# Optimization experiments

Hardware: AMD Instinct MI355X
Metric: run time of the kernel (lower is better)

Reference implementation:

```python
import jax, jax.numpy as jnp
import numpy as np

B_, L_, D_ = 2, 1024, 2048
E_, N_, R_, K_ = 4096, 16, 128, 4
EPS = 1e-5


def setup_inputs() -> dict:
    key = jax.random.key(0)
    ks = jax.random.split(key, 12)
    s = lambda i, shape, scale=0.02: jax.random.normal(ks[i], shape, jnp.float32) * scale
    # dt bias init as in the module: inv_dt = dt + log(-expm1(-dt)), dt ~ logU[1e-3, 0.1]
    dt = jnp.exp(jax.random.uniform(ks[10], (E_,)) * (np.log(0.1) - np.log(0.001)) + np.log(0.001))
    inv_dt = dt + jnp.log(-jnp.expm1(-dt))
    return {
        'resid': jax.random.normal(ks[0], (B_, L_, D_), jnp.float32),
        'norm_w': jnp.ones((D_,), jnp.float32),
        'skip_w': s(1, (E_, D_)),
        'in_w': s(2, (E_, D_)),
        'conv_w': s(3, (E_, K_), 0.2),
        'conv_b': jnp.zeros((E_,), jnp.float32),
        'wd1': s(4, (R_, E_)),
        'wd2': s(5, (E_, R_), R_ ** -0.5),
        'wd2_b': inv_dt,
        'wB': s(6, (N_, E_)),
        'wC': s(7, (N_, E_)),
        'A_log': jnp.log(jnp.broadcast_to(jnp.arange(1, N_ + 1, dtype=jnp.float32), (E_, N_))),
        'W_D': jnp.ones((E_,), jnp.float32),
        'out_w': s(8, (D_, E_)),
    }


def _forward(resid, norm_w, skip_w, in_w, conv_w, conv_b, wd1, wd2, wd2_b,
             wB, wC, A_log, W_D, out_w):
    B, L, D = resid.shape
    E, K = conv_w.shape
    N = A_log.shape[1]
    # RMSNorm
    rn = resid * jax.lax.rsqrt(jnp.mean(resid * resid, -1, keepdims=True) + EPS) * norm_w
    skip = rn @ skip_w.T                       # [B,L,E] gate branch (z)
    x_in = rn @ in_w.T                         # [B,L,E]
    # depthwise causal conv1d (pad left K-1, truncate to L), then SiLU
    xp = jnp.pad(x_in, ((0, 0), (K - 1, 0), (0, 0)))
    conv = conv_b + sum(xp[:, k:k + L, :] * conv_w[:, k] for k in range(K))
    x = jax.nn.silu(conv)                      # [B,L,E] ssm input
    # low-rank delta, input-dependent B/C
    delta = jax.nn.softplus((x @ wd1.T) @ wd2.T + wd2_b)   # [B,L,E]
    A = -jnp.exp(A_log)                        # [E,N]
    Bm = x @ wB.T                              # [B,L,N]
    Cm = x @ wC.T                              # [B,L,N]

    def step(h, inp):
        d_l, b_l, c_l, x_l = inp               # [B,E],[B,N],[B,N],[B,E]
        h = jnp.exp(d_l[:, :, None] * A) * h + (d_l * x_l)[:, :, None] * b_l[:, None, :]
        y_l = jnp.einsum('ben,bn->be', h, c_l)
        return h, y_l

    h0 = jnp.zeros((B, E, N), resid.dtype)
    xs = (delta.transpose(1, 0, 2), Bm.transpose(1, 0, 2),
          Cm.transpose(1, 0, 2), x.transpose(1, 0, 2))
    _, ys = jax.lax.scan(step, h0, xs)         # ys: [L,B,E]
    y = ys.transpose(1, 0, 2) + x * W_D        # skip connection via D
    y = y * jax.nn.silu(skip)                  # gating
    return resid + y @ out_w.T                 # out_proj + residual


def reference(resid, norm_w, skip_w, in_w, conv_w, conv_b, wd1, wd2, wd2_b,
              wB, wC, A_log, W_D, out_w):
    return _forward(resid, norm_w, skip_w, in_w, conv_w, conv_b, wd1, wd2,
                    wd2_b, wB, wC, A_log, W_D, out_w)
```

## Files before the change

kernel.cpp:

```cpp
#include <hip/hip_runtime.h>
#include <stdint.h>

#define NB 2
#define NL 1024
#define ND 2048
#define NE 4096
#define NN 16
#define NR 128
#define NKC 4
#define NBL (NB*NL)
#define EPSV 1e-5f
#define SEG_T 256
#define SCAN_T 32

typedef __attribute__((ext_vector_type(4))) float f32x4;
typedef __attribute__((ext_vector_type(8))) short short8;
typedef __attribute__((ext_vector_type(8))) unsigned short ushort8;
typedef __attribute__((ext_vector_type(4))) unsigned short ushort4_t;
typedef __attribute__((ext_vector_type(2))) unsigned short ushort2_t;

__device__ __forceinline__ unsigned short f2bf(float f) {
  union { float f; unsigned u; } v; v.f = f;
  unsigned r = v.u + 0x7FFFu + ((v.u >> 16) & 1u);
  return (unsigned short)(r >> 16);
}

__device__ __forceinline__ float bf2f(unsigned short u) {
  union { unsigned u; float f; } v; v.u = (unsigned)u << 16; return v.f;
}

__device__ __forceinline__ void load_lds16(const void* g, void* l) {
  __builtin_amdgcn_global_load_lds((const __attribute__((address_space(1))) void*)g,
                                   (__attribute__((address_space(3))) void*)l,
                                   16, 0, 0);
}

template<int CTRL>
__device__ __forceinline__ float dpp_mov(float v) {
  return __int_as_float(__builtin_amdgcn_update_dpp(
      0, __float_as_int(v), CTRL, 0xF, 0xF, true));
}

__global__ void rmsnorm_kernel(const float* __restrict__ resid,
                               const float* __restrict__ nw,
                               unsigned short* __restrict__ rn) {
  int row = blockIdx.x;
  int tid = threadIdx.x;
  const float* r = resid + (size_t)row * ND;
  f32x4 v0 = *(const f32x4*)(r + tid * 8);
  f32x4 v1 = *(const f32x4*)(r + tid * 8 + 4);
  float vals[8];
#pragma unroll
  for (int i = 0; i < 4; ++i) { vals[i] = v0[i]; vals[4 + i] = v1[i]; }
  float ss = 0.f;
#pragma unroll
  for (int i = 0; i < 8; ++i) ss += vals[i] * vals[i];
  for (int o = 32; o > 0; o >>= 1) ss += __shfl_down(ss, o);
  __shared__ float ps[4];
  if ((tid & 63) == 0) ps[tid >> 6] = ss;
  __syncthreads();
  float tot = ps[0] + ps[1] + ps[2] + ps[3];
  float scale = rsqrtf(tot / (float)ND + EPSV);
  ushort8 o8;
#pragma unroll
  for (int i = 0; i < 8; ++i) o8[i] = f2bf(vals[i] * scale * nw[tid * 8 + i]);
  *(ushort8*)(rn + (size_t)row * ND + tid * 8) = o8;
}

__global__ void cast_bf16_kernel(const float* __restrict__ in,
                                 unsigned short* __restrict__ out, int n8) {
  int i = blockIdx.x * blockDim.x + threadIdx.x;
  if (i >= n8) return;
  f32x4 a = *(const f32x4*)(in + (size_t)i * 8);
  f32x4 b = *(const f32x4*)(in + (size_t)i * 8 + 4);
  ushort8 o;
#pragma unroll
  for (int j = 0; j < 4; ++j) { o[j] = f2bf(a[j]); o[4 + j] = f2bf(b[j]); }
  *(ushort8*)(out + (size_t)i * 8) = o;
}

__global__ void build_wcat_kernel(const float* __restrict__ wd1,
                                  const float* __restrict__ wB,
                                  const float* __restrict__ wC,
                                  unsigned short* __restrict__ out) {
  int i = blockIdx.x * blockDim.x + threadIdx.x;
  if (i >= 256 * NE / 8) return;
  int col8 = i & (NE / 8 - 1);
  int row = i >> 9;
  const float* src = nullptr; int srow = 0;
  if (row < 128)      { src = wd1; srow = row; }
  else if (row < 144) { src = wB;  srow = row - 128; }
  else if (row < 160) { src = wC;  srow = row - 144; }
  ushort8 o;
  if (src) {
    f32x4 a = *(const f32x4*)(src + (size_t)srow * NE + col8 * 8);
    f32x4 b = *(const f32x4*)(src + (size_t)srow * NE + col8 * 8 + 4);
#pragma unroll
    for (int j = 0; j < 4; ++j) { o[j] = f2bf(a[j]); o[4 + j] = f2bf(b[j]); }
  } else {
#pragma unroll
    for (int j = 0; j < 8; ++j) o[j] = 0;
  }
  *(ushort8*)(out + (size_t)row * NE + col8 * 8) = o;
}

__global__ __launch_bounds__(512, 2)
void gemm256_fused(const unsigned short* __restrict__ A,
                   const unsigned short* __restrict__ B,
                   float* __restrict__ Gout,
                   unsigned short* __restrict__ Xout) {
  const int K = 2048, NH = K / 32;
  __shared__ unsigned short Asl[4][8192];
  __shared__ unsigned short Bsl[4][8192];
  int tid = threadIdx.x;
  int w = tid >> 6, lane = tid & 63;
  int wm = w >> 2, wn = w & 3;
  int lr = lane & 15, kg8 = (lane >> 4) * 8;
  int m0 = blockIdx.y * 256, n0 = blockIdx.x * 256;

  const unsigned short* ga = A + (size_t)(m0 + (tid >> 2)) * K + (tid & 3) * 8;
  const unsigned short* gb = B + (size_t)(n0 + (tid >> 2)) * K + (tid & 3) * 8;
  char* ldsA0 = (char*)&Asl[0][0] + w * 1024;
  char* ldsB0 = (char*)&Bsl[0][0] + w * 1024;

  auto stageA = [&](int h) {
    int slot = h & 3, k0 = h * 32;
    load_lds16(ga + k0, ldsA0 + slot * 16384);
    load_lds16(ga + k0 + (size_t)128 * K, ldsA0 + slot * 16384 + 8192);
  };
  auto stageB = [&](int h) {
    int slot = h & 3, k0 = h * 32;
    load_lds16(gb + k0, ldsB0 + slot * 16384);
    load_lds16(gb + k0 + (size_t)128 * K, ldsB0 + slot * 16384 + 8192);
  };

  f32x4 acc[8][4];
#pragma unroll
  for (int i = 0; i < 8; ++i)
#pragma unroll
    for (int j = 0; j < 4; ++j) acc[i][j] = (f32x4){0.f, 0.f, 0.f, 0.f};

  stageA(0); stageB(0); stageA(1); stageB(1); stageA(2); stageB(2);
  asm volatile("s_waitcnt vmcnt(8)" ::: "memory");
  __builtin_amdgcn_s_barrier();

  for (int h = 0; h < NH; ++h) {
    int slot = h & 3;
    const unsigned short* As_ = &Asl[slot][0];
    const unsigned short* Bs_ = &Bsl[slot][0];
    int arow = wm * 128 + lr;
    int brow = wn * 64 + lr;
    short8 a[8], b[4];
#pragma unroll
    for (int i = 0; i < 4; ++i)
      a[i] = *(const short8*)&As_[(arow + i * 16) * 32 + kg8];
#pragma unroll
    for (int j = 0; j < 4; ++j)
      b[j] = *(const short8*)&Bs_[(brow + j * 16) * 32 + kg8];
    if (h + 3 < NH) stageA(h + 3);
    __builtin_amdgcn_s_barrier();
    __builtin_amdgcn_s_setprio(1);
#pragma unroll
    for (int i = 0; i < 4; ++i)
#pragma unroll
      for (int j = 0; j < 4; ++j)
        acc[i][j] = __builtin_amdgcn_mfma_f32_16x16x32_bf16(a[i], b[j], acc[i][j], 0, 0, 0);
    __builtin_amdgcn_s_setprio(0);
    __builtin_amdgcn_s_barrier();
#pragma unroll
    for (int i = 0; i < 4; ++i)
      a[4 + i] = *(const short8*)&As_[(arow + (4 + i) * 16) * 32 + kg8];
    if (h + 3 < NH) stageB(h + 3);
    __builtin_amdgcn_s_barrier();
    __builtin_amdgcn_s_setprio(1);
#pragma unroll
    for (int i = 0; i < 4; ++i)
#pragma unroll
      for (int j = 0; j < 4; ++j)
        acc[4 + i][j] = __builtin_amdgcn_mfma_f32_16x16x32_bf16(a[4 + i], b[j], acc[4 + i][j], 0, 0, 0);
    __builtin_amdgcn_s_setprio(0);
    if (h < NH - 3)       { asm volatile("s_waitcnt vmcnt(8)" ::: "memory"); }
    else if (h == NH - 3) { asm volatile("s_waitcnt vmcnt(4)" ::: "memory"); }
    else if (h == NH - 2) { asm volatile("s_waitcnt vmcnt(0)" ::: "memory"); }
    __builtin_amdgcn_s_barrier();
  }

  int rbase = m0 + wm * 128 + (lane >> 4) * 4;
  int cbase = n0 + wn * 64 + (lane & 15);
  bool isg = (n0 < 4096);
#pragma unroll
  for (int mf = 0; mf < 8; ++mf) {
#pragma unroll
    for (int nf = 0; nf < 4; ++nf) {
      int col = cbase + nf * 16;
#pragma unroll
      for (int rr = 0; rr < 4; ++rr) {
        int row = rbase + mf * 16 + rr;
        float v = acc[mf][nf][rr];
        if (isg) Gout[(size_t)row * 4096 + col] = v / (1.f + __expf(-v));
        else     Xout[(size_t)row * 4096 + (col - 4096)] = f2bf(v);
      }
    }
  }
}

template<int MODE>
__global__ __launch_bounds__(256)
void gemm_bt(const unsigned short* __restrict__ A,
             const unsigned short* __restrict__ B,
             float* __restrict__ C,
             int M, int N, int K, int ksteps_per_z,
             const float* __restrict__ bias,
             const float* __restrict__ add) {
  __shared__ unsigned short As[4][128 * 32];
  __shared__ unsigned short Bs[4][128 * 32];
  int tid = threadIdx.x;
  int w = tid >> 6, lane = tid & 63;
  int m0 = blockIdx.y * 128, n0 = blockIdx.x * 128;
  int kz0 = blockIdx.z * ksteps_per_z * 32;
  if (MODE == 0) C += (size_t)blockIdx.z * M * N;
  const int NH = ksteps_per_z;

  f32x4 acc[4][4];
#pragma unroll
  for (int i = 0; i < 4; ++i)
#pragma unroll
    for (int j = 0; j < 4; ++j) acc[i][j] = (f32x4){0.f, 0.f, 0.f, 0.f};

  int wm = w >> 1, wn = w & 1;
  int lr = lane & 15, kg = lane >> 4;

  int fe0 = (w) * 512 + lane * 8;
  int fe1 = (4 + w) * 512 + lane * 8;
  int r0 = fe0 >> 5, c0 = fe0 & 31;
  int r1 = fe1 >> 5, c1 = fe1 & 31;
  const unsigned short* Ag0 = A + (size_t)(m0 + r0) * K + c0 + kz0;
  const unsigned short* Ag1 = A + (size_t)(m0 + r1) * K + c1 + kz0;
  const unsigned short* Bg0 = B + (size_t)(n0 + r0) * K + c0 + kz0;
  const unsigned short* Bg1 = B + (size_t)(n0 + r1) * K + c1 + kz0;

  auto stage = [&](int h) {
    int slot = h & 3, kk = h * 32;
    load_lds16(Ag0 + kk, &As[slot][(w) * 512]);
    load_lds16(Ag1 + kk, &As[slot][(4 + w) * 512]);
    load_lds16(Bg0 + kk, &Bs[slot][(w) * 512]);
    load_lds16(Bg1 + kk, &Bs[slot][(4 + w) * 512]);
  };

  stage(0);
  if (NH > 1) stage(1);
  if (NH > 2) stage(2);

  for (int h = 0; h < NH; ++h) {
    int slot = h & 3;
    __builtin_amdgcn_s_barrier();
    if (h + 3 < NH) stage(h + 3);
    int rem = NH - 1 - h; if (rem > 3) rem = 3;
    if (rem == 3)      { asm volatile("s_waitcnt vmcnt(12)" ::: "memory"); }
    else if (rem == 2) { asm volatile("s_waitcnt vmcnt(8)"  ::: "memory"); }
    else if (rem == 1) { asm volatile("s_waitcnt vmcnt(4)"  ::: "memory"); }
    else               { asm volatile("s_waitcnt vmcnt(0)"  ::: "memory"); }
    __builtin_amdgcn_s_barrier();
    short8 a[4], b[4];
#pragma unroll
    for (int i = 0; i < 4; ++i)
      a[i] = *(const short8*)&As[slot][(wm * 64 + i * 16 + lr) * 32 + kg * 8];
#pragma unroll
    for (int j = 0; j < 4; ++j)
      b[j] = *(const short8*)&Bs[slot][(wn * 64 + j * 16 + lr) * 32 + kg * 8];
    __builtin_amdgcn_s_setprio(1);
#pragma unroll
    for (int i = 0; i < 4; ++i)
#pragma unroll
      for (int j = 0; j < 4; ++j)
        acc[i][j] = __builtin_amdgcn_mfma_f32_16x16x32_bf16(a[i], b[j], acc[i][j], 0, 0, 0);
    __builtin_amdgcn_s_setprio(0);
  }

#pragma unroll
  for (int i = 0; i < 4; ++i) {
#pragma unroll
    for (int j = 0; j < 4; ++j) {
      int rbase = m0 + wm * 64 + i * 16 + kg * 4;
      int col = n0 + wn * 64 + j * 16 + lr;
#pragma unroll
      for (int r = 0; r < 4; ++r) {
        float v = acc[i][j][r];
        size_t idx = (size_t)(rbase + r) * N + col;
        if (MODE == 0) {
          C[idx] = v;
        } else if (MODE == 1) {
          float t = v + bias[col];
          ((unsigned short*)C)[idx] = f2bf((t > 20.f) ? t : log1pf(__expf(t)));
        } else {
          C[idx] = v + add[idx];
        }
      }
    }
  }
}

__global__ void conv_silu_kernel(const unsigned short* __restrict__ xin,
                                 const float* __restrict__ cw,
                                 const float* __restrict__ cb,
                                 unsigned short* __restrict__ xbf) {
  size_t idx = (size_t)blockIdx.x * blockDim.x + threadIdx.x;
  if (idx >= (size_t)NB * NL * NE) return;
  int e = (int)(idx & (NE - 1));
  int r = (int)(idx >> 12);
  int l = r & (NL - 1);
  float acc = cb[e];
#pragma unroll
  for (int k = 0; k < NKC; ++k) {
    int ls = l - 3 + k;
    if (ls >= 0) acc += bf2f(xin[(size_t)(r - 3 + k) * NE + e]) * cw[e * 4 + k];
  }
  float s = acc / (1.f + __expf(-acc));
  xbf[idx] = f2bf(s);
}

__global__ void reduce_tcat_kernel(const float* __restrict__ part,
                                   unsigned short* __restrict__ tbf,
                                   float* __restrict__ bc) {
  int idx = blockIdx.x * blockDim.x + threadIdx.x;
  if (idx >= NBL * 160) return;
  int m = idx / 160, c = idx - m * 160;
  float s = 0.f;
#pragma unroll
  for (int z = 0; z < 8; ++z) s += part[(size_t)z * NBL * 256 + (size_t)m * 256 + c];
  if (c < 128) tbf[m * 128 + c] = f2bf(s);
  else if (c < 144) bc[m * 32 + (c - 128)] = s;
  else bc[m * 32 + 16 + (c - 144)] = s;
}

__global__ __launch_bounds__(256)
void scan1_kernel(const unsigned short* __restrict__ delta_bf,
                  const unsigned short* __restrict__ x_bf,
                  const float* __restrict__ bc,
                  const float* __restrict__ gf,
                  const float* __restrict__ A_log,
                  const float* __restrict__ W_D,
                  unsigned short* __restrict__ yg,
                  float* __restrict__ fin,
                  float* __restrict__ dtot) {
  __shared__ unsigned short dxl[2][SCAN_T][2][16];
  __shared__ float gl[2][SCAN_T][16];
  __shared__ float BCl[2][SCAN_T][32];
  __shared__ float yl2[SCAN_T][16][2];
  __shared__ float wdl[16];
  int tid = threadIdx.x;
  int n = tid & 15, el = tid >> 4;
  int w = tid >> 6, lane = tid & 63;
  int e0 = blockIdx.x * 16;
  int b = blockIdx.y >> 2, seg = blockIdx.y & 3;
  int e = e0 + el;
  float A2 = -__expf(A_log[e * 16 + n]) * 1.44269504f;
  if (tid < 16) wdl[tid] = W_D[e0 + tid];
  float h = 0.f, cum = 0.f;

  const unsigned short* gdl = delta_bf + (size_t)b * NL * NE + e0;
  const unsigned short* gx  = x_bf + (size_t)b * NL * NE + e0;
  const float* gg  = gf + (size_t)b * NL * 4096 + e0;
  const float* gBC = bc + (size_t)b * NL * 32;

  const unsigned short* dxsrc = ((lane >> 1) & 1) ? gx : gdl;
  int dxrow = (w & 1) * 16 + (lane >> 2);
  int dxcol = (lane & 1) * 8;
  int grow = (w & 1) * 16 + (lane >> 2);
  int gcol = (lane & 3) * 4;
  int bcrow = w * 8 + (lane >> 3);
  int bccol = (lane & 7) * 4;
  int nloads = (seg == 0 || w < 2) ? 2 : 1;

  auto stage = [&](int buf, int c) {
    int l0 = seg * SEG_T + c * SCAN_T;
    if (w < 2)
      load_lds16(dxsrc + (size_t)(l0 + dxrow) * NE + dxcol, &dxl[buf][(w & 1) * 16][0][0]);
    else if (seg == 0)
      load_lds16(gg + (size_t)(l0 + grow) * 4096 + gcol, &gl[buf][(w & 1) * 16][0]);
    load_lds16(gBC + (size_t)(l0 + bcrow) * 32 + bccol, &BCl[buf][w * 8][0]);
  };

  stage(0, 0);
  const int nch = SEG_T / SCAN_T;
  for (int c = 0; c < nch; ++c) {
    int cur = c & 1;
    if (c + 1 < nch) {
      stage(cur ^ 1, c + 1);
      if (nloads == 2) { asm volatile("s_waitcnt vmcnt(2)" ::: "memory"); }
      else             { asm volatile("s_waitcnt vmcnt(1)" ::: "memory"); }
    } else {
      asm volatile("s_waitcnt vmcnt(0)" ::: "memory");
    }
    __syncthreads();
    const unsigned short (*dxc)[2][16] = dxl[cur];
    const float (*BCc)[32] = BCl[cur];
#pragma unroll 8
    for (int t = 0; t < SCAN_T; ++t) {
      float dc = bf2f(dxc[t][0][el]);
      float xc = bf2f(dxc[t][1][el]);
      float Bc = BCc[t][n];
      float Cc = BCc[t][16 + n];
      cum += dc;
      float a = dc * A2, ed;
      asm("v_exp_f32 %0, %1" : "=v"(ed) : "v"(a));
      h = ed * h + (dc * xc) * Bc;
      float p = h * Cc;
      p += dpp_mov<0xB1>(p);
      p += dpp_mov<0x4E>(p);
      p += dpp_mov<0x141>(p);
      if ((n & 7) == 0) yl2[t][el][n >> 3] = p;
    }
    __syncthreads();
    {
      int t = tid >> 3, part = tid & 7;
      int l0 = seg * SEG_T + c * SCAN_T;
      ushort2_t o;
#pragma unroll
      for (int j = 0; j < 2; ++j) {
        int ee = part * 2 + j;
        float xv = bf2f(dxc[t][1][ee]);
        float y = yl2[t][ee][0] + yl2[t][ee][1] + xv * wdl[ee];
        if (seg == 0) y *= gl[cur][t][ee];
        o[j] = f2bf(y);
      }
      *(ushort2_t*)(yg + (size_t)(b * NL + l0 + t) * NE + e0 + part * 2) = o;
    }
    __syncthreads();
  }
  fin[(size_t)((seg * 2 + b) * 4096 + e) * 16 + n] = h;
  if (n == 0) dtot[(size_t)(seg * 2 + b) * 4096 + e] = cum;
}

__global__ __launch_bounds__(256)
void scan2_kernel(const unsigned short* __restrict__ delta_bf,
                  unsigned short* __restrict__ yg,
                  const float* __restrict__ bc,
                  const float* __restrict__ gf,
                  const float* __restrict__ A_log,
                  const float* __restrict__ fin,
                  const float* __restrict__ dtot) {
  __shared__ unsigned short dl[2][SCAN_T][16];
  __shared__ unsigned short ypl[2][SCAN_T][16];
  __shared__ float Cl[2][SCAN_T][16];
  __shared__ float gl2[2][SCAN_T][16];
  __shared__ float ycl[SCAN_T][16][2];
  int tid = threadIdx.x;
  int n = tid & 15, el = tid >> 4;
  int w = tid >> 6, lane = tid & 63;
  int e0 = blockIdx.x * 16;
  int b = blockIdx.y / 3, seg = 1 + blockIdx.y % 3;
  int e = e0 + el;
  float A2 = -__expf(A_log[e * 16 + n]) * 1.44269504f;
  float h = fin[(size_t)(b * 4096 + e) * 16 + n];
  for (int s2 = 1; s2 < seg; ++s2) {
    float dt = dtot[(size_t)(s2 * 2 + b) * 4096 + e];
    float a = A2 * dt, pw;
    asm("v_exp_f32 %0, %1" : "=v"(pw) : "v"(a));
    h = fin[(size_t)((s2 * 2 + b) * 4096 + e) * 16 + n] + pw * h;
  }

  const unsigned short* gd = delta_bf + (size_t)b * NL * NE + e0;
  unsigned short* gy = yg + (size_t)b * NL * NE + e0;
  const float* gg  = gf + (size_t)b * NL * 4096 + e0;
  const float* gBC = bc + (size_t)b * NL * 32;

  int dyrow = lane >> 1;
  int dycol = (lane & 1) * 8;
  int crow = (w & 1) * 16 + (lane >> 2);
  int ccol = 16 + (lane & 3) * 4;
  int grow = (w & 1) * 16 + (lane >> 2);
  int gcol = (lane & 3) * 4;
  int nloads = (w < 2) ? 2 : 1;

  auto stage = [&](int buf, int c) {
    int l0 = seg * SEG_T + c * SCAN_T;
    if (w == 0)      load_lds16(gd + (size_t)(l0 + dyrow) * NE + dycol, &dl[buf][0][0]);
    else if (w == 1) load_lds16(gy + (size_t)(l0 + dyrow) * NE + dycol, &ypl[buf][0][0]);
    if (w < 2) load_lds16(gBC + (size_t)(l0 + crow) * 32 + ccol, &Cl[buf][(w & 1) * 16][0]);
    else       load_lds16(gg + (size_t)(l0 + grow) * 4096 + gcol, &gl2[buf][(w & 1) * 16][0]);
  };

  stage(0, 0);
  float cum = 0.f;
  const int nch = SEG_T / SCAN_T;
  for (int c = 0; c < nch; ++c) {
    int cur = c & 1;
    if (c + 1 < nch) {
      stage(cur ^ 1, c + 1);
      if (nloads == 2) { asm volatile("s_waitcnt vmcnt(2)" ::: "memory"); }
      else             { asm volatile("s_waitcnt vmcnt(1)" ::: "memory"); }
    } else {
      asm volatile("s_waitcnt vmcnt(0)" ::: "memory");
    }
    __syncthreads();
    const unsigned short (*dc_)[16] = dl[cur];
    const float (*Cc_)[16] = Cl[cur];
#pragma unroll 8
    for (int t = 0; t < SCAN_T; ++t) {
      float dcv = bf2f(dc_[t][el]);
      cum += dcv;
      float a = A2 * cum, pw;
      asm("v_exp_f32 %0, %1" : "=v"(pw) : "v"(a));
      float p = (pw * h) * Cc_[t][n];
      p += dpp_mov<0xB1>(p);
      p += dpp_mov<0x4E>(p);
      p += dpp_mov<0x141>(p);
      if ((n & 7) == 0) ycl[t][el][n >> 3] = p;
    }
    __syncthreads();
    {
      int t = tid >> 3, part = tid & 7;
      int l0 = seg * SEG_T + c * SCAN_T;
      ushort2_t o;
#pragma unroll
      for (int j = 0; j < 2; ++j) {
        int ee = part * 2 + j;
        float y = ycl[t][ee][0] + ycl[t][ee][1] + bf2f(ypl[cur][t][ee]);
        o[j] = f2bf(y * gl2[cur][t][ee]);
      }
      *(ushort2_t*)(gy + (size_t)(l0 + t) * NE + part * 2) = o;
    }
    __syncthreads();
  }
}

extern "C" void kernel_launch(void* const* d_in, const int* in_sizes, int n_in,
                              void* d_out, int out_size, void* d_ws, size_t ws_size,
                              hipStream_t stream) {
  const float* resid  = (const float*)d_in[0];
  const float* norm_w = (const float*)d_in[1];
  const float* skip_w = (const float*)d_in[2];
  const float* in_w   = (const float*)d_in[3];
  const float* conv_w = (const float*)d_in[4];
  const float* conv_b = (const float*)d_in[5];
  const float* wd1    = (const float*)d_in[6];
  const float* wd2    = (const float*)d_in[7];
  const float* wd2_b  = (const float*)d_in[8];
  const float* wB     = (const float*)d_in[9];
  const float* wC     = (const float*)d_in[10];
  const float* A_log  = (const float*)d_in[11];
  const float* W_D    = (const float*)d_in[12];
  const float* out_w  = (const float*)d_in[13];
  float* out = (float*)d_out;

  char* ws = (char*)d_ws;
  size_t off = 0;
  auto alloc = [&](size_t bytes) -> void* {
    void* p = ws + off;
    off += (bytes + 255) & ~(size_t)255;
    return p;
  };
  unsigned short* rn_bf      = (unsigned short*)alloc((size_t)NBL * ND * 2);
  unsigned short* wskipin_bf = (unsigned short*)alloc((size_t)2 * NE * ND * 2);
  unsigned short* wout_bf    = (unsigned short*)alloc((size_t)ND * NE * 2);
  unsigned short* wd2_bf     = (unsigned short*)alloc((size_t)NE * NR * 2);
  unsigned short* wcat_bf    = (unsigned short*)alloc((size_t)256 * NE * 2);
  float* g_f                 = (float*)alloc((size_t)NBL * NE * 4);
  unsigned short* xin_bf     = (unsigned short*)alloc((size_t)NBL * NE * 2);
  unsigned short* x_bf       = (unsigned short*)alloc((size_t)NBL * NE * 2);
  float* part_f              = (float*)alloc((size_t)8 * NBL * 256 * 4);
  unsigned short* t_bf       = (unsigned short*)alloc((size_t)NBL * NR * 2);
  float* bc_f                = (float*)alloc((size_t)NBL * 32 * 4);
  unsigned short* yg_bf      = (unsigned short*)alloc((size_t)NBL * NE * 2);
  float* fin_f               = (float*)alloc((size_t)4 * NB * NE * 16 * 4);
  float* dtot_f              = (float*)alloc((size_t)4 * NB * NE * 4);
  unsigned short* delta_bf = wskipin_bf;
  (void)ws_size; (void)in_sizes; (void)n_in; (void)out_size;

  rmsnorm_kernel<<<dim3(NBL), dim3(256), 0, stream>>>(resid, norm_w, rn_bf);

  cast_bf16_kernel<<<dim3((NE * ND / 8 + 255) / 256), dim3(256), 0, stream>>>(skip_w, wskipin_bf, NE * ND / 8);
  cast_bf16_kernel<<<dim3((NE * ND / 8 + 255) / 256), dim3(256), 0, stream>>>(in_w, wskipin_bf + (size_t)NE * ND, NE * ND / 8);
  cast_bf16_kernel<<<dim3((ND * NE / 8 + 255) / 256), dim3(256), 0, stream>>>(out_w, wout_bf, ND * NE / 8);
  cast_bf16_kernel<<<dim3((NE * NR / 8 + 255) / 256), dim3(256), 0, stream>>>(wd2, wd2_bf, NE * NR / 8);
  build_wcat_kernel<<<dim3(256 * NE / 8 / 256), dim3(256), 0, stream>>>(wd1, wB, wC, wcat_bf);

  gemm256_fused<<<dim3(8192 / 256, NBL / 256), dim3(512), 0, stream>>>(
      rn_bf, wskipin_bf, g_f, xin_bf);

  conv_silu_kernel<<<dim3((int)(((size_t)NB * NL * NE) / 256)), dim3(256), 0, stream>>>(
      xin_bf, conv_w, conv_b, x_bf);

  gemm_bt<0><<<dim3(256 / 128, NBL / 128, 8), dim3(256), 0, stream>>>(
      x_bf, wcat_bf, part_f, NBL, 256, NE, (NE / 32) / 8, nullptr, nullptr);
  reduce_tcat_kernel<<<dim3((NBL * 160 + 255) / 256), dim3(256), 0, stream>>>(
      part_f, t_bf, bc_f);

  gemm_bt<1><<<dim3(NE / 128, NBL / 128, 1), dim3(256), 0, stream>>>(
      t_bf, wd2_bf, (float*)delta_bf, NBL, NE, NR, NR / 32, wd2_b, nullptr);

  scan1_kernel<<<dim3(NE / 16, NB * 4), dim3(256), 0, stream>>>(
      delta_bf, x_bf, bc_f, g_f, A_log, W_D, yg_bf, fin_f, dtot_f);
  scan2_kernel<<<dim3(NE / 16, NB * 3), dim3(256), 0, stream>>>(
      delta_bf, yg_bf, bc_f, g_f, A_log, fin_f, dtot_f);

  gemm_bt<2><<<dim3(ND / 128, NBL / 128, 1), dim3(256), 0, stream>>>(
      yg_bf, wout_bf, out, NBL, ND, NE, NE / 32, nullptr, resid);
}
```

Measured before the change: 419.3 us.

## Split-K the output projection and x-projection GEMMs, shrink LDS pipeline to 3 stages

The out_proj GEMM now uses split-K by 4, writing partials into the g_f buffer that is dead after the scans, and a new vectorized reduce kernel adds them to resid. The previous launch had only 256 blocks, so splitting K raises occupancy on the many-CU GPU. The x-projection GEMM split-K goes from 8 to 16, and the GEMM LDS ring drops from 4 to 3 stages to cut shared memory per block. The cost is extra partial-sum traffic, with about 67MB written and read back for the out projection, and a shallower prefetch depth.

```diff
diff --git a/kernel.cpp b/kernel.cpp
--- a/kernel.cpp
+++ b/kernel.cpp
@@ -210,10 +210,9 @@
              const unsigned short* __restrict__ B,
              float* __restrict__ C,
              int M, int N, int K, int ksteps_per_z,
-             const float* __restrict__ bias,
-             const float* __restrict__ add) {
-  __shared__ unsigned short As[4][128 * 32];
-  __shared__ unsigned short Bs[4][128 * 32];
+             const float* __restrict__ bias) {
+  __shared__ unsigned short As[3][128 * 32];
+  __shared__ unsigned short Bs[3][128 * 32];
   int tid = threadIdx.x;
   int w = tid >> 6, lane = tid & 63;
   int m0 = blockIdx.y * 128, n0 = blockIdx.x * 128;
@@ -240,7 +239,7 @@
   const unsigned short* Bg1 = B + (size_t)(n0 + r1) * K + c1 + kz0;
 
   auto stage = [&](int h) {
-    int slot = h & 3, kk = h * 32;
+    int slot = h % 3, kk = h * 32;
     load_lds16(Ag0 + kk, &As[slot][(w) * 512]);
     load_lds16(Ag1 + kk, &As[slot][(4 + w) * 512]);
     load_lds16(Bg0 + kk, &Bs[slot][(w) * 512]);
@@ -249,17 +248,15 @@
 
   stage(0);
   if (NH > 1) stage(1);
-  if (NH > 2) stage(2);
 
   for (int h = 0; h < NH; ++h) {
-    int slot = h & 3;
+    int slot = h % 3;
     __builtin_amdgcn_s_barrier();
-    if (h + 3 < NH) stage(h + 3);
-    int rem = NH - 1 - h; if (rem > 3) rem = 3;
-    if (rem == 3)      { asm volatile("s_waitcnt vmcnt(12)" ::: "memory"); }
-    else if (rem == 2) { asm volatile("s_waitcnt vmcnt(8)"  ::: "memory"); }
-    else if (rem == 1) { asm volatile("s_waitcnt vmcnt(4)"  ::: "memory"); }
-    else               { asm volatile("s_waitcnt vmcnt(0)"  ::: "memory"); }
+    if (h + 2 < NH) stage(h + 2);
+    int rem = NH - 1 - h;
+    if (rem >= 2)      { asm volatile("s_waitcnt vmcnt(8)" ::: "memory"); }
+    else if (rem == 1) { asm volatile("s_waitcnt vmcnt(4)" ::: "memory"); }
+    else               { asm volatile("s_waitcnt vmcnt(0)" ::: "memory"); }
     __builtin_amdgcn_s_barrier();
     short8 a[4], b[4];
 #pragma unroll
@@ -289,15 +286,25 @@
         size_t idx = (size_t)(rbase + r) * N + col;
         if (MODE == 0) {
           C[idx] = v;
-        } else if (MODE == 1) {
+        } else {
           float t = v + bias[col];
           ((unsigned short*)C)[idx] = f2bf((t > 20.f) ? t : log1pf(__expf(t)));
-        } else {
-          C[idx] = v + add[idx];
         }
       }
     }
   }
+}
+
+__global__ void reduce_out_kernel(const float* __restrict__ part,
+                                  const float* __restrict__ resid,
+                                  float* __restrict__ out) {
+  size_t base = ((size_t)blockIdx.x * blockDim.x + threadIdx.x) * 4;
+  if (base >= (size_t)NBL * ND) return;
+  f32x4 r = *(const f32x4*)(resid + base);
+#pragma unroll
+  for (int z = 0; z < 4; ++z)
+    r += *(const f32x4*)(part + (size_t)z * NBL * ND + base);
+  *(f32x4*)(out + base) = r;
 }
 
 __global__ void conv_silu_kernel(const unsigned short* __restrict__ xin,
@@ -327,7 +334,7 @@
   int m = idx / 160, c = idx - m * 160;
   float s = 0.f;
 #pragma unroll
-  for (int z = 0; z < 8; ++z) s += part[(size_t)z * NBL * 256 + (size_t)m * 256 + c];
+  for (int z = 0; z < 16; ++z) s += part[(size_t)z * NBL * 256 + (size_t)m * 256 + c];
   if (c < 128) tbf[m * 128 + c] = f2bf(s);
   else if (c < 144) bc[m * 32 + (c - 128)] = s;
   else bc[m * 32 + 16 + (c - 144)] = s;
@@ -559,13 +566,14 @@
   float* g_f                 = (float*)alloc((size_t)NBL * NE * 4);
   unsigned short* xin_bf     = (unsigned short*)alloc((size_t)NBL * NE * 2);
   unsigned short* x_bf       = (unsigned short*)alloc((size_t)NBL * NE * 2);
-  float* part_f              = (float*)alloc((size_t)8 * NBL * 256 * 4);
+  float* part_f              = (float*)alloc((size_t)16 * NBL * 256 * 4);
   unsigned short* t_bf       = (unsigned short*)alloc((size_t)NBL * NR * 2);
   float* bc_f                = (float*)alloc((size_t)NBL * 32 * 4);
   unsigned short* yg_bf      = (unsigned short*)alloc((size_t)NBL * NE * 2);
   float* fin_f               = (float*)alloc((size_t)4 * NB * NE * 16 * 4);
   float* dtot_f              = (float*)alloc((size_t)4 * NB * NE * 4);
   unsigned short* delta_bf = wskipin_bf;
+  float* part2_f = g_f;
   (void)ws_size; (void)in_sizes; (void)n_in; (void)out_size;
 
   rmsnorm_kernel<<<dim3(NBL), dim3(256), 0, stream>>>(resid, norm_w, rn_bf);
@@ -582,19 +590,21 @@
   conv_silu_kernel<<<dim3((int)(((size_t)NB * NL * NE) / 256)), dim3(256), 0, stream>>>(
       xin_bf, conv_w, conv_b, x_bf);
 
-  gemm_bt<0><<<dim3(256 / 128, NBL / 128, 8), dim3(256), 0, stream>>>(
-      x_bf, wcat_bf, part_f, NBL, 256, NE, (NE / 32) / 8, nullptr, nullptr);
+  gemm_bt<0><<<dim3(256 / 128, NBL / 128, 16), dim3(256), 0, stream>>>(
+      x_bf, wcat_bf, part_f, NBL, 256, NE, (NE / 32) / 16, nullptr);
   reduce_tcat_kernel<<<dim3((NBL * 160 + 255) / 256), dim3(256), 0, stream>>>(
       part_f, t_bf, bc_f);
 
   gemm_bt<1><<<dim3(NE / 128, NBL / 128, 1), dim3(256), 0, stream>>>(
-      t_bf, wd2_bf, (float*)delta_bf, NBL, NE, NR, NR / 32, wd2_b, nullptr);
+      t_bf, wd2_bf, (float*)delta_bf, NBL, NE, NR, NR / 32, wd2_b);
 
   scan1_kernel<<<dim3(NE / 16, NB * 4), dim3(256), 0, stream>>>(
       delta_bf, x_bf, bc_f, g_f, A_log, W_D, yg_bf, fin_f, dtot_f);
   scan2_kernel<<<dim3(NE / 16, NB * 3), dim3(256), 0, stream>>>(
       delta_bf, yg_bf, bc_f, g_f, A_log, fin_f, dtot_f);
 
-  gemm_bt<2><<<dim3(ND / 128, NBL / 128, 1), dim3(256), 0, stream>>>(
-      yg_bf, wout_bf, out, NBL, ND, NE, NE / 32, nullptr, resid);
-}
+  gemm_bt<0><<<dim3(ND / 128, NBL / 128, 4), dim3(256), 0, stream>>>(
+      yg_bf, wout_bf, part2_f, NBL, ND, NE, (NE / 32) / 4, nullptr);
+  reduce_out_kernel<<<dim3((int)((size_t)NBL * ND / 4 / 256)), dim3(256), 0, stream>>>(
+      part2_f, resid, out);
+}
```

Result: no change. 411.6 us (-1.8%).
